# Performance work log

Hardware: AMD Instinct MI355X
Metric: run time of the kernel (lower is better)

The kernel has to match this reference:

```python
import jax, jax.numpy as jnp
import numpy as np

INPUT_SIZE = 256
OUTPUT_SIZE = 128
N = 8192
SLOPE = 0.01
NEG_BIG = -9e15


def setup_inputs() -> dict:
    key = jax.random.key(0)
    k_h, k_adj, k_W, k_a = jax.random.split(key, 4)
    h = jax.random.normal(k_h, (N, INPUT_SIZE), dtype=jnp.float32)
    adj = jax.random.randint(k_adj, (N, N), 0, 2, dtype=jnp.int32)
    # xavier_uniform with gain=1.414
    gain = 1.414
    lim_W = gain * np.sqrt(6.0 / (INPUT_SIZE + OUTPUT_SIZE))
    W = jax.random.uniform(k_W, (INPUT_SIZE, OUTPUT_SIZE), dtype=jnp.float32, minval=-lim_W, maxval=lim_W)
    lim_a = gain * np.sqrt(6.0 / (2 * OUTPUT_SIZE + 1))
    a = jax.random.uniform(k_a, (2 * OUTPUT_SIZE, 1), dtype=jnp.float32, minval=-lim_a, maxval=lim_a)
    return {"h": h, "adj": adj, "W": W, "a": a}


def reference(h, adj, W, a):
    # Wh: [N, F]
    Wh = h @ W
    Fo = Wh.shape[1]
    # Original builds [N, N, 2F] concat then matmul with a; equivalent to
    # e[i, j] = leaky_relu(Wh[i] . a[:F] + Wh[j] . a[F:]) via broadcasting.
    src = Wh @ a[:Fo, 0]   # [N]
    dst = Wh @ a[Fo:, 0]   # [N]
    e = jax.nn.leaky_relu(src[:, None] + dst[None, :], negative_slope=SLOPE)  # [N, N]
    att = jnp.where(adj > 0, e, NEG_BIG)
    att = jax.nn.softmax(att, axis=1)
    return att @ Wh
```

## Files before the change

### kernel.cpp

```cpp
#include <hip/hip_runtime.h>
#include <hip/hip_bf16.h>

typedef unsigned short u16;
typedef unsigned char u8;
typedef unsigned int u32;
typedef __attribute__((ext_vector_type(8))) short short8;
typedef __attribute__((ext_vector_type(4))) float f32x4;

#define NN 8192
#define KIN 256
#define FOUT 128
#define SPLITS 8
#define KPER (NN / SPLITS)
#define KSTEPS (KPER / 32)
#define L2E 1.4426950408889634f

__device__ __forceinline__ float exp2fast(float x) { return __builtin_amdgcn_exp2f(x); }

__device__ __forceinline__ u16 f2bf(float f) {
    u32 u = __float_as_uint(f);
    u32 r = ((u >> 16) & 1u) + 0x7fffu;
    return (u16)((u + r) >> 16);
}
__device__ __forceinline__ u32 pk_bf16(float a, float b) {
    union { __hip_bfloat162 h2; u32 u; } cv;
    cv.h2 = __float22bfloat162_rn(make_float2(a, b));
    return cv.u;
}
__device__ __forceinline__ u32 fkey(float f) {
    u32 b = __float_as_uint(f);
    return (b & 0x80000000u) ? ~b : (b | 0x80000000u);
}
__device__ __forceinline__ float funkey(u32 k) {
    u32 b = (k & 0x80000000u) ? (k & 0x7fffffffu) : ~k;
    return __uint_as_float(b);
}

__global__ __launch_bounds__(256) void k0_pack(const int* __restrict__ adj,
                                              u8* __restrict__ bm)
{
    size_t idx = (size_t)blockIdx.x * 256 + threadIdx.x;
    int4 v = *(const int4*)(adj + idx * 4);
    bm[idx] = (u8)((v.x > 0) | ((v.y > 0) << 1) | ((v.z > 0) << 2) | ((v.w > 0) << 3));
}

__global__ __launch_bounds__(256) void k1_wh(
    const float* __restrict__ h, const float* __restrict__ W, const float* __restrict__ a,
    u16* __restrict__ whfrag,
    float* __restrict__ src, float* __restrict__ dl2e, u32* __restrict__ gmaxk)
{
    __shared__ float hT[64][36];
    __shared__ u16   lt[128][40];
    __shared__ float sd[32][2];
    const int t  = threadIdx.x;
    const int m0 = blockIdx.x * 32;
    const int rq = t >> 5, cq = t & 31;

    float acc[4][4];
#pragma unroll
    for (int i = 0; i < 4; i++)
#pragma unroll
        for (int j = 0; j < 4; j++) acc[i][j] = 0.f;
    if (t < 64) sd[t >> 1][t & 1] = 0.f;

    for (int kt = 0; kt < KIN; kt += 64) {
        __syncthreads();
#pragma unroll
        for (int s2 = 0; s2 < 2; s2++) {
            int f = s2 * 256 + t;
            int r = f >> 4, kc = (f & 15) * 4;
            float4 hv = *(const float4*)(h + (size_t)(m0 + r) * KIN + kt + kc);
            hT[kc + 0][r] = hv.x; hT[kc + 1][r] = hv.y;
            hT[kc + 2][r] = hv.z; hT[kc + 3][r] = hv.w;
        }
        __syncthreads();
        for (int k = 0; k < 64; k++) {
            float4 wv = *(const float4*)(W + (size_t)(kt + k) * FOUT + cq * 4);
            float h0 = hT[k][rq * 4 + 0], h1 = hT[k][rq * 4 + 1];
            float h2 = hT[k][rq * 4 + 2], h3 = hT[k][rq * 4 + 3];
            acc[0][0] += h0 * wv.x; acc[0][1] += h0 * wv.y; acc[0][2] += h0 * wv.z; acc[0][3] += h0 * wv.w;
            acc[1][0] += h1 * wv.x; acc[1][1] += h1 * wv.y; acc[1][2] += h1 * wv.z; acc[1][3] += h1 * wv.w;
            acc[2][0] += h2 * wv.x; acc[2][1] += h2 * wv.y; acc[2][2] += h2 * wv.z; acc[2][3] += h2 * wv.w;
            acc[3][0] += h3 * wv.x; acc[3][1] += h3 * wv.y; acc[3][2] += h3 * wv.z; acc[3][3] += h3 * wv.w;
        }
    }
#pragma unroll
    for (int i = 0; i < 4; i++) {
        float sp = 0.f, dp = 0.f;
#pragma unroll
        for (int j = 0; j < 4; j++) {
            sp += acc[i][j] * a[cq * 4 + j];
            dp += acc[i][j] * a[FOUT + cq * 4 + j];
            lt[cq * 4 + j][rq * 4 + i] = f2bf(acc[i][j]);
        }
        atomicAdd(&sd[rq * 4 + i][0], sp);
        atomicAdd(&sd[rq * 4 + i][1], dp);
    }
    __syncthreads();
    if (t < 32) { src[m0 + t] = sd[t][0]; dl2e[m0 + t] = sd[t][1] * L2E; }
    if (t < 64) {
        float v = (t < 32) ? sd[t][1] : -3.0e38f;
#pragma unroll
        for (int off = 32; off >= 1; off >>= 1) v = fmaxf(v, __shfl_down(v, off));
        if (t == 0) atomicMax(gmaxk, fkey(v));
    }
    const int kstep = blockIdx.x;
#pragma unroll
    for (int p = 0; p < 2; p++) {
        int f = p * 256 + t;
        int nt = f >> 6;
        int l  = f & 63;
        short8 v = *(const short8*)&lt[nt * 16 + (l & 15)][(l >> 4) * 8];
        *(short8*)(whfrag + ((size_t)(kstep * 8 + nt) * 64 + l) * 8) = v;
    }
}

__global__ __launch_bounds__(256, 4) void k2_attn(
    const u8* __restrict__ bm, const float* __restrict__ src, const float* __restrict__ dl2e,
    const u16* __restrict__ whfrag, const u32* __restrict__ gmaxk,
    float* __restrict__ accp, float* __restrict__ lp)
{
    __shared__ u16 Pall[4][16][40];
    const int t = threadIdx.x;
    const int lane = t & 63, wave = t >> 6;
    u16 (*P)[40] = Pall[wave];
    const int strip = blockIdx.x * 4 + wave;
    const int i0 = strip * 16;
    const int split = blockIdx.y;
    const int l15 = lane & 15, quad = lane >> 4;
    const int r0 = lane >> 3;
    const int r1 = 8 + r0;
    const int co = (lane & 7) * 4;

    const float gm = funkey(*gmaxk) * L2E;
    float s0 = src[i0 + r0] * L2E, s1 = src[i0 + r1] * L2E;
    float xm0 = s0 + gm, xm1 = s1 + gm;
    float C0 = fmaxf(xm0, 0.01f * xm0), C1 = fmaxf(xm1, 0.01f * xm1);
    const float y10 = s0 - C0, y20 = 0.01f * s0 - C0;
    const float y11 = s1 - C1, y21 = 0.01f * s1 - C1;

    const u8* brow0 = bm + (size_t)(i0 + r0) * (NN / 4) + (lane & 7);
    const u8* brow1 = bm + (size_t)(i0 + r1) * (NN / 4) + (lane & 7);
    const int st0 = blockIdx.x & (KSTEPS - 1);
    const int kbase = split * KPER;

    f32x4 acc[8];
#pragma unroll
    for (int nt = 0; nt < 8; nt++) acc[nt] = {0.f, 0.f, 0.f, 0.f};
    float ps0 = 0.f, ps1 = 0.f;

    u32 n0s[2], n1s[2]; float4 dvs[2];
#pragma unroll
    for (int s = 0; s < 2; s++) {
        int kb = kbase + ((st0 + s) & (KSTEPS - 1)) * 32;
        n0s[s] = brow0[kb >> 2];
        n1s[s] = brow1[kb >> 2];
        dvs[s] = *(const float4*)(dl2e + kb + co);
    }

#pragma unroll 4
    for (int it = 0; it < KSTEPS; ++it) {
        const int sl = it & 1;
        const int kb = kbase + ((st0 + it) & (KSTEPS - 1)) * 32;

        uint4 bv[8];
        const u16* wf = whfrag + ((size_t)(kb >> 5) * 8 * 64 + lane) * 8;
#pragma unroll
        for (int nt = 0; nt < 8; nt++)
            bv[nt] = *(const uint4*)(wf + (size_t)nt * 64 * 8);

        u32 n0 = n0s[sl], n1 = n1s[sl];
        float4 d = dvs[sl];
        {
            float x, p0, p1, p2, p3;
            x = fmaxf(y10 + d.x, y20 + 0.01f * d.x); p0 = exp2fast((n0 & 1u) ? x : -1.0e9f);
            x = fmaxf(y10 + d.y, y20 + 0.01f * d.y); p1 = exp2fast((n0 & 2u) ? x : -1.0e9f);
            x = fmaxf(y10 + d.z, y20 + 0.01f * d.z); p2 = exp2fast((n0 & 4u) ? x : -1.0e9f);
            x = fmaxf(y10 + d.w, y20 + 0.01f * d.w); p3 = exp2fast((n0 & 8u) ? x : -1.0e9f);
            ps0 += (p0 + p1) + (p2 + p3);
            *(uint2*)&P[r0][co] = make_uint2(pk_bf16(p0, p1), pk_bf16(p2, p3));
            x = fmaxf(y11 + d.x, y21 + 0.01f * d.x); p0 = exp2fast((n1 & 1u) ? x : -1.0e9f);
            x = fmaxf(y11 + d.y, y21 + 0.01f * d.y); p1 = exp2fast((n1 & 2u) ? x : -1.0e9f);
            x = fmaxf(y11 + d.z, y21 + 0.01f * d.z); p2 = exp2fast((n1 & 4u) ? x : -1.0e9f);
            x = fmaxf(y11 + d.w, y21 + 0.01f * d.w); p3 = exp2fast((n1 & 8u) ? x : -1.0e9f);
            ps1 += (p0 + p1) + (p2 + p3);
            *(uint2*)&P[r1][co] = make_uint2(pk_bf16(p0, p1), pk_bf16(p2, p3));
        }

        {
            int kb2 = kbase + ((st0 + it + 2) & (KSTEPS - 1)) * 32;
            n0s[sl] = brow0[kb2 >> 2];
            n1s[sl] = brow1[kb2 >> 2];
            dvs[sl] = *(const float4*)(dl2e + kb2 + co);
        }

        short8 af = *(const short8*)&P[l15][quad * 8];

#pragma unroll
        for (int nt = 0; nt < 8; nt++) {
            union { uint4 q; short8 s8; } bf; bf.q = bv[nt];
            acc[nt] = __builtin_amdgcn_mfma_f32_16x16x32_bf16(af, bf.s8, acc[nt], 0, 0, 0);
        }
    }

    ps0 += __shfl_down(ps0, 4, 8); ps0 += __shfl_down(ps0, 2, 8); ps0 += __shfl_down(ps0, 1, 8);
    ps1 += __shfl_down(ps1, 4, 8); ps1 += __shfl_down(ps1, 2, 8); ps1 += __shfl_down(ps1, 1, 8);
    if ((lane & 7) == 0) {
        lp[split * NN + i0 + r0] = ps0;
        lp[split * NN + i0 + r1] = ps1;
    }

    float* ab = accp + (size_t)split * (NN * FOUT);
#pragma unroll
    for (int nt = 0; nt < 8; nt++)
        *(f32x4*)&ab[((size_t)(strip * 8 + nt) * 64 + lane) * 4] = acc[nt];
}

__global__ __launch_bounds__(256) void k2b_rsum(const float* __restrict__ lp,
                                               float* __restrict__ rinv)
{
    int i = blockIdx.x * 256 + threadIdx.x;
    float s = 0.f;
#pragma unroll
    for (int sp = 0; sp < SPLITS; sp++) s += lp[sp * NN + i];
    rinv[i] = 1.0f / s;
}

__global__ __launch_bounds__(256) void k3_comb(
    const float* __restrict__ accp, const float* __restrict__ rinv, float* __restrict__ out)
{
    int idx = blockIdx.x * 256 + threadIdx.x;
    int tile = idx >> 6, l = idx & 63;
    float4 s = make_float4(0.f, 0.f, 0.f, 0.f);
#pragma unroll
    for (int sp = 0; sp < SPLITS; sp++) {
        float4 v = *(const float4*)(accp + (size_t)sp * (NN * FOUT) + (size_t)idx * 4);
        s.x += v.x; s.y += v.y; s.z += v.z; s.w += v.w;
    }
    int row0 = (tile >> 3) * 16 + (l >> 4) * 4;
    int col  = (tile & 7) * 16 + (l & 15);
    float4 ri = *(const float4*)(rinv + row0);
    out[(size_t)(row0 + 0) * FOUT + col] = s.x * ri.x;
    out[(size_t)(row0 + 1) * FOUT + col] = s.y * ri.y;
    out[(size_t)(row0 + 2) * FOUT + col] = s.z * ri.z;
    out[(size_t)(row0 + 3) * FOUT + col] = s.w * ri.w;
}

extern "C" void kernel_launch(void* const* d_in, const int* in_sizes, int n_in,
                              void* d_out, int out_size, void* d_ws, size_t ws_size,
                              hipStream_t stream) {
    const float* h   = (const float*)d_in[0];
    const int*   adj = (const int*)d_in[1];
    const float* W   = (const float*)d_in[2];
    const float* a   = (const float*)d_in[3];
    float* out = (float*)d_out;

    char* ws = (char*)d_ws;
    u16*   whfrag = (u16*)ws;
    float* src    = (float*)(ws + (2u << 20));
    float* dl2e   = src + NN;
    u32*   gmaxk  = (u32*)(dl2e + NN);
    float* accp   = (float*)(ws + (3u << 20));
    float* lp     = (float*)(ws + (35u << 20));
    float* rinv   = (float*)(ws + (36u << 20));
    u8*    bm     = (u8*)(ws + (37u << 20));

    (void)hipMemsetAsync(gmaxk, 0, sizeof(u32), stream);
    k0_pack<<<dim3((NN / 4) * (NN / 256)), dim3(256), 0, stream>>>(adj, bm);
    k1_wh<<<dim3(NN / 32), dim3(256), 0, stream>>>(h, W, a, whfrag, src, dl2e, gmaxk);
    k2_attn<<<dim3(NN / 64, SPLITS), dim3(256), 0, stream>>>(bm, src, dl2e, whfrag, gmaxk, accp, lp);
    k2b_rsum<<<dim3(NN / 256), dim3(256), 0, stream>>>(lp, rinv);
    k3_comb<<<dim3((NN * FOUT / 4) / 256), dim3(256), 0, stream>>>(accp, rinv, out);
}
```

Baseline: 463.6 us.

## Fuse adjacency packing, attention and split reduction into one kernel

The separate adjacency bit-packing kernel and the split-K partial-sum and combine kernels are removed. Each block now handles 16 rows, with its four waves splitting the 8192 columns. Each wave packs its own adjacency slice into shared memory. The waves then reduce their partial accumulators and row sums through shared memory and write normalized output directly. This drops the round trip of the packed mask and the large partial-accumulator buffer through global memory, and it drops kernel launches. In exchange, the adjacency loads are no longer software-prefetched, there are fewer blocks (512), and the large shared-memory allocation may reduce occupancy.

```diff
diff --git a/kernel.cpp b/kernel.cpp
--- a/kernel.cpp
+++ b/kernel.cpp
@@ -10,9 +10,7 @@
 #define NN 8192
 #define KIN 256
 #define FOUT 128
-#define SPLITS 8
-#define KPER (NN / SPLITS)
-#define KSTEPS (KPER / 32)
+#define KW 2048
 #define L2E 1.4426950408889634f
 
 __device__ __forceinline__ float exp2fast(float x) { return __builtin_amdgcn_exp2f(x); }
@@ -34,14 +32,6 @@
 __device__ __forceinline__ float funkey(u32 k) {
     u32 b = (k & 0x80000000u) ? (k & 0x7fffffffu) : ~k;
     return __uint_as_float(b);
-}
-
-__global__ __launch_bounds__(256) void k0_pack(const int* __restrict__ adj,
-                                              u8* __restrict__ bm)
-{
-    size_t idx = (size_t)blockIdx.x * 256 + threadIdx.x;
-    int4 v = *(const int4*)(adj + idx * 4);
-    bm[idx] = (u8)((v.x > 0) | ((v.y > 0) << 1) | ((v.z > 0) << 2) | ((v.w > 0) << 3));
 }
 
 __global__ __launch_bounds__(256) void k1_wh(
@@ -116,21 +106,30 @@
 }
 
 __global__ __launch_bounds__(256, 4) void k2_attn(
-    const u8* __restrict__ bm, const float* __restrict__ src, const float* __restrict__ dl2e,
+    const int* __restrict__ adj, const float* __restrict__ src, const float* __restrict__ dl2e,
     const u16* __restrict__ whfrag, const u32* __restrict__ gmaxk,
-    float* __restrict__ accp, float* __restrict__ lp)
+    float* __restrict__ out)
 {
+    __shared__ u8  mask[4][16][512];
     __shared__ u16 Pall[4][16][40];
     const int t = threadIdx.x;
     const int lane = t & 63, wave = t >> 6;
-    u16 (*P)[40] = Pall[wave];
-    const int strip = blockIdx.x * 4 + wave;
-    const int i0 = strip * 16;
-    const int split = blockIdx.y;
+    const int i0 = blockIdx.x * 16;
     const int l15 = lane & 15, quad = lane >> 4;
-    const int r0 = lane >> 3;
-    const int r1 = 8 + r0;
+    const int r0 = lane >> 3, r1 = 8 + r0;
     const int co = (lane & 7) * 4;
+    const int cbase = wave * KW;
+
+#pragma unroll
+    for (int r = 0; r < 16; r++) {
+        const int* ap = adj + (size_t)(i0 + r) * NN + cbase;
+#pragma unroll
+        for (int c = 0; c < 8; c++) {
+            int4 v = *(const int4*)(ap + c * 256 + lane * 4);
+            mask[wave][r][c * 64 + lane] =
+                (u8)((v.x > 0) | ((v.y > 0) << 1) | ((v.z > 0) << 2) | ((v.w > 0) << 3));
+        }
+    }
 
     const float gm = funkey(*gmaxk) * L2E;
     float s0 = src[i0 + r0] * L2E, s1 = src[i0 + r1] * L2E;
@@ -139,38 +138,24 @@
     const float y10 = s0 - C0, y20 = 0.01f * s0 - C0;
     const float y11 = s1 - C1, y21 = 0.01f * s1 - C1;
 
-    const u8* brow0 = bm + (size_t)(i0 + r0) * (NN / 4) + (lane & 7);
-    const u8* brow1 = bm + (size_t)(i0 + r1) * (NN / 4) + (lane & 7);
-    const int st0 = blockIdx.x & (KSTEPS - 1);
-    const int kbase = split * KPER;
-
+    u16 (*P)[40] = Pall[wave];
     f32x4 acc[8];
 #pragma unroll
     for (int nt = 0; nt < 8; nt++) acc[nt] = {0.f, 0.f, 0.f, 0.f};
     float ps0 = 0.f, ps1 = 0.f;
 
-    u32 n0s[2], n1s[2]; float4 dvs[2];
-#pragma unroll
-    for (int s = 0; s < 2; s++) {
-        int kb = kbase + ((st0 + s) & (KSTEPS - 1)) * 32;
-        n0s[s] = brow0[kb >> 2];
-        n1s[s] = brow1[kb >> 2];
-        dvs[s] = *(const float4*)(dl2e + kb + co);
-    }
-
-#pragma unroll 4
-    for (int it = 0; it < KSTEPS; ++it) {
-        const int sl = it & 1;
-        const int kb = kbase + ((st0 + it) & (KSTEPS - 1)) * 32;
+    for (int kk = 0; kk < 64; ++kk) {
+        const int kb = cbase + kk * 32;
 
         uint4 bv[8];
-        const u16* wf = whfrag + ((size_t)(kb >> 5) * 8 * 64 + lane) * 8;
+        const u16* wf = whfrag + ((size_t)((kb >> 5) * 8) * 64 + lane) * 8;
 #pragma unroll
         for (int nt = 0; nt < 8; nt++)
             bv[nt] = *(const uint4*)(wf + (size_t)nt * 64 * 8);
 
-        u32 n0 = n0s[sl], n1 = n1s[sl];
-        float4 d = dvs[sl];
+        u32 n0 = mask[wave][r0][kk * 8 + (lane & 7)];
+        u32 n1 = mask[wave][r1][kk * 8 + (lane & 7)];
+        float4 d = *(const float4*)(dl2e + kb + co);
         {
             float x, p0, p1, p2, p3;
             x = fmaxf(y10 + d.x, y20 + 0.01f * d.x); p0 = exp2fast((n0 & 1u) ? x : -1.0e9f);
@@ -187,13 +172,6 @@
             *(uint2*)&P[r1][co] = make_uint2(pk_bf16(p0, p1), pk_bf16(p2, p3));
         }
 
-        {
-            int kb2 = kbase + ((st0 + it + 2) & (KSTEPS - 1)) * 32;
-            n0s[sl] = brow0[kb2 >> 2];
-            n1s[sl] = brow1[kb2 >> 2];
-            dvs[sl] = *(const float4*)(dl2e + kb2 + co);
-        }
-
         short8 af = *(const short8*)&P[l15][quad * 8];
 
 #pragma unroll
@@ -205,45 +183,41 @@
 
     ps0 += __shfl_down(ps0, 4, 8); ps0 += __shfl_down(ps0, 2, 8); ps0 += __shfl_down(ps0, 1, 8);
     ps1 += __shfl_down(ps1, 4, 8); ps1 += __shfl_down(ps1, 2, 8); ps1 += __shfl_down(ps1, 1, 8);
-    if ((lane & 7) == 0) {
-        lp[split * NN + i0 + r0] = ps0;
-        lp[split * NN + i0 + r1] = ps1;
-    }
-
-    float* ab = accp + (size_t)split * (NN * FOUT);
-#pragma unroll
-    for (int nt = 0; nt < 8; nt++)
-        *(f32x4*)&ab[((size_t)(strip * 8 + nt) * 64 + lane) * 4] = acc[nt];
-}
-
-__global__ __launch_bounds__(256) void k2b_rsum(const float* __restrict__ lp,
-                                               float* __restrict__ rinv)
-{
-    int i = blockIdx.x * 256 + threadIdx.x;
-    float s = 0.f;
-#pragma unroll
-    for (int sp = 0; sp < SPLITS; sp++) s += lp[sp * NN + i];
-    rinv[i] = 1.0f / s;
-}
-
-__global__ __launch_bounds__(256) void k3_comb(
-    const float* __restrict__ accp, const float* __restrict__ rinv, float* __restrict__ out)
-{
-    int idx = blockIdx.x * 256 + threadIdx.x;
-    int tile = idx >> 6, l = idx & 63;
-    float4 s = make_float4(0.f, 0.f, 0.f, 0.f);
-#pragma unroll
-    for (int sp = 0; sp < SPLITS; sp++) {
-        float4 v = *(const float4*)(accp + (size_t)sp * (NN * FOUT) + (size_t)idx * 4);
-        s.x += v.x; s.y += v.y; s.z += v.z; s.w += v.w;
-    }
-    int row0 = (tile >> 3) * 16 + (l >> 4) * 4;
-    int col  = (tile & 7) * 16 + (l & 15);
-    float4 ri = *(const float4*)(rinv + row0);
-    out[(size_t)(row0 + 0) * FOUT + col] = s.x * ri.x;
-    out[(size_t)(row0 + 1) * FOUT + col] = s.y * ri.y;
-    out[(size_t)(row0 + 2) * FOUT + col] = s.z * ri.z;
-    out[(size_t)(row0 + 3) * FOUT + col] = s.w * ri.w;
+    float* pf = (float*)&Pall[wave][0][0];
+    if ((lane & 7) == 0) { pf[r0] = ps0; pf[r1] = ps1; }
+
+    float* ex = (float*)&mask[wave][0][0];
+    {
+        int crow = quad * 4, ccol = l15;
+#pragma unroll
+        for (int nt = 0; nt < 8; nt++)
+#pragma unroll
+            for (int reg = 0; reg < 4; reg++)
+                ex[(crow + reg) * FOUT + nt * 16 + ccol] = acc[nt][reg];
+    }
+    __syncthreads();
+
+    {
+        int row = t >> 4, c8 = (t & 15) * 8;
+        float s[8];
+#pragma unroll
+        for (int j = 0; j < 8; j++) s[j] = 0.f;
+        float l = 0.f;
+#pragma unroll
+        for (int w = 0; w < 4; w++) {
+            const float* exw = (const float*)&mask[w][0][0];
+            const float* pfw = (const float*)&Pall[w][0][0];
+            float4 v0 = *(const float4*)&exw[row * FOUT + c8];
+            float4 v1 = *(const float4*)&exw[row * FOUT + c8 + 4];
+            s[0] += v0.x; s[1] += v0.y; s[2] += v0.z; s[3] += v0.w;
+            s[4] += v1.x; s[5] += v1.y; s[6] += v1.z; s[7] += v1.w;
+            l += pfw[row];
+        }
+        float ri = 1.0f / l;
+        float* op = out + (size_t)(i0 + row) * FOUT + c8;
+        *(float4*)op       = make_float4(s[0] * ri, s[1] * ri, s[2] * ri, s[3] * ri);
+        *(float4*)(op + 4) = make_float4(s[4] * ri, s[5] * ri, s[6] * ri, s[7] * ri);
+    }
 }
 
 extern "C" void kernel_launch(void* const* d_in, const int* in_sizes, int n_in,
@@ -260,15 +234,8 @@
     float* src    = (float*)(ws + (2u << 20));
     float* dl2e   = src + NN;
     u32*   gmaxk  = (u32*)(dl2e + NN);
-    float* accp   = (float*)(ws + (3u << 20));
-    float* lp     = (float*)(ws + (35u << 20));
-    float* rinv   = (float*)(ws + (36u << 20));
-    u8*    bm     = (u8*)(ws + (37u << 20));
 
     (void)hipMemsetAsync(gmaxk, 0, sizeof(u32), stream);
-    k0_pack<<<dim3((NN / 4) * (NN / 256)), dim3(256), 0, stream>>>(adj, bm);
     k1_wh<<<dim3(NN / 32), dim3(256), 0, stream>>>(h, W, a, whfrag, src, dl2e, gmaxk);
-    k2_attn<<<dim3(NN / 64, SPLITS), dim3(256), 0, stream>>>(bm, src, dl2e, whfrag, gmaxk, accp, lp);
-    k2b_rsum<<<dim3(NN / 256), dim3(256), 0, stream>>>(lp, rinv);
-    k3_comb<<<dim3((NN * FOUT / 4) / 256), dim3(256), 0, stream>>>(accp, rinv, out);
-}
+    k2_attn<<<dim3(NN / 16), dim3(256), 0, stream>>>(adj, src, dl2e, whfrag, gmaxk, out);
+}
```

Measured after the change: 486.0 us. +4.8%, slower.
